# Kernel optimization log

Hardware: AMD Instinct MI355X
Metric: run time of the kernel (lower is better)

Reference implementation:

```python
import jax, jax.numpy as jnp
import numpy as np
from jax.scipy.special import logsumexp

TEMPERATURE = 0.1
BETA = 0.999
EPS = 1e-8
HARD_K = 10  # min(num_classes // 4, 10) with num_classes = 1000


def _l2norm(x, axis=-1):
    return x * jax.lax.rsqrt(jnp.sum(x * x, axis=axis, keepdims=True) + 1e-24)


def setup_inputs() -> dict:
    key = jax.random.key(0)
    k1, k2, k3, k4, k5 = jax.random.split(key, 5)
    B, D, C, M = 4096, 1024, 1000, 32768
    return {
        "image_features": jax.random.normal(k1, (B, D), dtype=jnp.float32),
        "prompts": jax.random.normal(k2, (C, D), dtype=jnp.float32),
        "labels": jax.random.randint(k3, (B, C), 0, 2, dtype=jnp.int32),
        "memory_features": jax.random.normal(k4, (M, D), dtype=jnp.float32),
        "memory_labels": jax.random.randint(k5, (M, C), 0, 2, dtype=jnp.int32),
        "mem_ptr": 16384,
    }


def reference(image_features, prompts, labels, memory_features, memory_labels, mem_ptr):
    B, D = image_features.shape
    C = prompts.shape[0]
    labels_f = labels.astype(jnp.float32)

    # z_img = F.normalize(image_features)
    z_img = _l2norm(image_features, axis=1)

    # class weights (effective-number reweighting), computed from this batch's labels
    counts = labels_f.sum(axis=0)                              # [C]
    effective_num = 1.0 - jnp.power(jnp.float32(BETA), counts)
    weights = (1.0 - BETA) / (effective_num + EPS)
    weights = weights / jnp.sum(weights) * C                   # [C]

    # memory bank update (detached write of current batch at ptr), then use [:ptr+B]
    mem_f = memory_features.at[mem_ptr:mem_ptr + B].set(jax.lax.stop_gradient(z_img))
    mem_l = memory_labels.at[mem_ptr:mem_ptr + B].set(labels)
    used = mem_ptr + B  # static

    enhanced_features = jnp.concatenate([z_img, mem_f[:used]], axis=0)     # [N, D]
    enhanced_labels = jnp.concatenate([labels_f, mem_l[:used].astype(jnp.float32)], axis=0)  # [N, C]

    z_prompts = _l2norm(prompts, axis=1)                       # [C, D]
    sim = (enhanced_features @ z_prompts.T) / TEMPERATURE      # [N, C]

    pos_mask = enhanced_labels > 0                             # [N, C]

    # hard negatives: top-K similarities among negatives define the keep threshold
    sim_for_neg = jnp.where(pos_mask, -jnp.inf, sim)
    hard_neg_vals, _ = jax.lax.top_k(sim_for_neg, HARD_K)      # [N, K]
    min_hard_neg = hard_neg_vals[:, -1:]                       # [N, 1]
    neg_mask = (~pos_mask) & (sim >= min_hard_neg)
    full_mask = pos_mask | neg_mask

    lse = logsumexp(jnp.where(full_mask, sim, -jnp.inf), axis=1)  # [N]
    log_prob = sim - lse[:, None]                              # [N, C]

    posf = pos_mask.astype(sim.dtype)
    pos_w = posf * weights[None, :]                            # [N, C]
    weight_sums = pos_w.sum(axis=1)                            # [N]
    loss_num = (pos_w * (-log_prob)).sum(axis=1)               # [N]

    valid = weight_sums > 0
    loss_per_sample = jnp.where(valid, loss_num / (weight_sums + EPS), 0.0)
    n_valid = jnp.maximum(valid.sum(), 1)
    attr_loss = loss_per_sample.sum() / n_valid.astype(sim.dtype)
    # single attribute -> total_loss / num_valid_attrs == attr_loss
    return attr_loss
```

## Files before the change

### kernel.cpp

```cpp
#include <hip/hip_runtime.h>
#include <math.h>

#define BN    4096
#define DD    1024
#define CC    1000
#define MM    32768
#define ROWS_CAP 32768


#define NGROUP_A 512
#define NGROUP_B 16
#define NCOUNT   512
#define NBITS    512

#define NSUB 32

typedef __attribute__((ext_vector_type(8))) int   int8v;
typedef __attribute__((ext_vector_type(16))) float f32x16;

__device__ __forceinline__ float wave_sum_f(float v) {
#pragma unroll
  for (int off = 32; off >= 1; off >>= 1) v += __shfl_xor(v, off, 64);
  return v;
}

__device__ __forceinline__ int pack4(float a, float b, float c, float d) {
  int p = __builtin_amdgcn_cvt_pk_fp8_f32(a, b, 0, false);
  p = __builtin_amdgcn_cvt_pk_fp8_f32(c, d, p, true);
  return p;
}

__device__ __forceinline__ void gload16(const unsigned char* g, unsigned char* l) {
  __builtin_amdgcn_global_load_lds(
      (const __attribute__((address_space(1))) unsigned int*)g,
      (__attribute__((address_space(3))) unsigned int*)l, 16, 0, 0);
}

__device__ __forceinline__ void ins10(float* t, float v) {
#pragma unroll
  for (int i = 9; i >= 1; --i) t[i] = __builtin_amdgcn_fmed3f(v, t[i - 1], t[i]);
  t[0] = fmaxf(t[0], v);
}

__global__ __launch_bounds__(256) void conv_kernel(const float* __restrict__ img,
                                                   const float* __restrict__ prompts,
                                                   const float* __restrict__ mem,
                                                   const int* __restrict__ memptr,
                                                   unsigned char* __restrict__ A,
                                                   unsigned char* __restrict__ B,
                                                   const int* __restrict__ labels,
                                                   const int* __restrict__ mlabels,
                                                   int* __restrict__ counts,
                                                   unsigned* __restrict__ bitmask) {
  const int blk = blockIdx.x;
  const int t = threadIdx.x;
  const int lane = t & 63;
  const int wid = t >> 6;
  const int nrows = BN + memptr[0];
  const int padded = (nrows + 127) & ~127;

  if (blk >= NGROUP_A + NGROUP_B + NCOUNT) {
    const int bi = blk - (NGROUP_A + NGROUP_B + NCOUNT);
    const int rowBase = bi * 64;
    if (rowBase >= padded) return;
    for (int i = 0; i < 16; ++i) {
      const int row = rowBase + wid * 16 + i;
      if (row >= padded) continue;
      unsigned bits = 0;
      if (row < nrows) {
        const int* lr = (row < BN) ? labels + (size_t)row * CC
                                   : mlabels + (size_t)(row - BN) * CC;
        const int cbase = lane * 16;
#pragma unroll
        for (int g = 0; g < 4; ++g) {
          int c = cbase + g * 4;
          int4 l4;
          if (c + 3 < CC) l4 = *(const int4*)(lr + c);
          else {
            l4.x = (c < CC) ? lr[c] : 0;
            l4.y = (c + 1 < CC) ? lr[c + 1] : 0;
            l4.z = (c + 2 < CC) ? lr[c + 2] : 0;
            l4.w = (c + 3 < CC) ? lr[c + 3] : 0;
          }
          unsigned m = 0;
          if (l4.x > 0) m |= 1u;
          if (l4.y > 0) m |= 2u;
          if (l4.z > 0) m |= 4u;
          if (l4.w > 0) m |= 8u;
          bits |= m << (g * 4);
        }
      }
      unsigned pair = __shfl_xor(bits, 1, 64);
      if (!(lane & 1)) bitmask[(size_t)row * 32 + (lane >> 1)] = bits | (pair << 16);
    }
    return;
  }

  if (blk >= NGROUP_A + NGROUP_B) {
    const int ci = blk - (NGROUP_A + NGROUP_B);
    const int c = (ci & 3) * 256 + t;
    if (c >= CC) return;
    const int b0 = (ci >> 2) * 32;
    int s = 0;
#pragma unroll
    for (int b = 0; b < 32; ++b) s += labels[(size_t)(b0 + b) * CC + c];
    atomicAdd(&counts[c], s);
    return;
  }

  __shared__ unsigned char tile[65536];

  const bool isB = (blk >= NGROUP_A);
  const int g = isB ? (blk - NGROUP_A) : blk;
  const int rowBase = g * 64;
  if (!isB && rowBase >= padded) return;

  unsigned char* dstBase = (isB ? B : A)
      + (size_t)(rowBase >> 7) * 131072 + (size_t)(rowBase & 64) * 16;

  for (int i = 0; i < 16; ++i) {
    const int r = wid * 16 + i;
    const int row = rowBase + r;
    const float* src = nullptr;
    float esc = 1.0f;
    bool needNorm = false;
    if (isB) {
      if (row < CC) { src = prompts + (size_t)row * DD; needNorm = true; esc = 10.0f; }
    } else {
      if (row < BN)         { src = img + (size_t)row * DD; needNorm = true; }
      else if (row < nrows) { src = mem + (size_t)(row - BN) * DD; }
    }
    int4 o = {0, 0, 0, 0};
    if (src) {
      const float4* s4 = (const float4*)src + lane * 4;
      float4 a = s4[0], b = s4[1], c = s4[2], d = s4[3];
      float sc = esc;
      if (needNorm) {
        float ss = a.x * a.x + a.y * a.y + a.z * a.z + a.w * a.w
                 + b.x * b.x + b.y * b.y + b.z * b.z + b.w * b.w
                 + c.x * c.x + c.y * c.y + c.z * c.z + c.w * c.w
                 + d.x * d.x + d.y * d.y + d.z * d.z + d.w * d.w;
        ss = wave_sum_f(ss);
        sc = esc * rsqrtf(ss + 1e-24f);
      }
      o.x = pack4(a.x * sc, a.y * sc, a.z * sc, a.w * sc);
      o.y = pack4(b.x * sc, b.y * sc, b.z * sc, b.w * sc);
      o.z = pack4(c.x * sc, c.y * sc, c.z * sc, c.w * sc);
      o.w = pack4(d.x * sc, d.y * sc, d.z * sc, d.w * sc);
    }
    *(int4*)(tile + lane * 1024 + (((r + lane) & 63) << 4)) = o;
  }
  __syncthreads();

#pragma unroll
  for (int p = 0; p < 16; ++p) {
    const int ochunk = p * 256 + t;
    const int kc = ochunk >> 6;
    const int rl = ochunk & 63;
    int4 v = *(const int4*)(tile + kc * 1024 + (((rl + kc) & 63) << 4));
    *(int4*)(dstBase + (size_t)kc * 2048 + rl * 16) = v;
  }
}

__global__ __launch_bounds__(512) void gemm_fused(
    const unsigned char* __restrict__ A, const unsigned char* __restrict__ Bm,
    const unsigned* __restrict__ bitmask, const int* __restrict__ counts,
    const int* __restrict__ memptr, float* __restrict__ partials) {
  const int f = blockIdx.x;
  const int x = f & 7;
  const int s = f >> 3;
  const int cb = s & 7;
  const int rt = (s >> 3) * 8 + x;

  const int nrows = BN + memptr[0];
  const int row0 = rt * 128;
  if (row0 >= nrows) return;
  const int c0 = cb * 128;

  __shared__ unsigned char As[2][16384];
  __shared__ unsigned char Bs[2][16384];
  __shared__ unsigned posbits[128][4];
  __shared__ float wcol[128];
  __shared__ float wpart[8];

  const int t = threadIdx.x;
  const int lane = t & 63;
  const int wid = t >> 6;
  const int wm = (wid >> 1) * 32;
  const int wn = (wid & 1) * 64;
  const int q = lane >> 5;
  const int rr = lane & 31;

  const unsigned char* gaT = A + (size_t)row0 * DD;
  const unsigned char* gbT = Bm + (size_t)c0 * DD;

#pragma unroll
  for (int p = 0; p < 2; ++p) {
    gload16(gaT + p * 8192 + t * 16, As[0] + p * 8192 + t * 16);
    gload16(gbT + p * 8192 + t * 16, Bs[0] + p * 8192 + t * 16);
  }

  {
    float wv[2];
    float accw = 0.f;
#pragma unroll
    for (int i = 0; i < 2; ++i) {
      int c = t + i * 512;
      float w = 0.f;
      if (c < CC) {
        float cnt = (float)counts[c];
        float en = 1.0f - expf(cnt * logf(0.999f));
        w = (1.0f - 0.999f) / (en + 1e-8f);
      }
      wv[i] = w;
      accw += w;
    }
    float sw = wave_sum_f(accw);
    if (lane == 0) wpart[wid] = sw;
    if (t < 128) {
      const int4 bm = *(const int4*)(bitmask + (size_t)(row0 + t) * 32 + cb * 4);
      posbits[t][0] = bm.x; posbits[t][1] = bm.y;
      posbits[t][2] = bm.z; posbits[t][3] = bm.w;
    }
    __syncthreads();
    float tot = 0.f;
#pragma unroll
    for (int i = 0; i < 8; ++i) tot += wpart[i];
    float scw = (float)CC / tot;
#pragma unroll
    for (int i = 0; i < 2; ++i) {
      int c = t + i * 512;
      if (c >= c0 && c < c0 + 128) wcol[c - c0] = wv[i] * scw;
    }
  }

  f32x16 acc[2] = {};

  int cur = 0;
  for (int it = 0; it < 8; ++it) {
    if (it < 7) {
      const size_t kb = (size_t)(it + 1) * 16384;
#pragma unroll
      for (int p = 0; p < 2; ++p) {
        gload16(gaT + kb + p * 8192 + t * 16, As[cur ^ 1] + p * 8192 + t * 16);
        gload16(gbT + kb + p * 8192 + t * 16, Bs[cur ^ 1] + p * 8192 + t * 16);
      }
    }
#pragma unroll
    for (int h = 0; h < 2; ++h) {
      const int kc = h * 4 + q * 2;
      int8v af, bfv[2];
      {
        const unsigned char* pa = As[cur] + kc * 2048 + (wm + rr) * 16;
        int4 lo4 = *(const int4*)pa;
        int4 hi4 = *(const int4*)(pa + 2048);
        af[0] = lo4.x; af[1] = lo4.y; af[2] = lo4.z; af[3] = lo4.w;
        af[4] = hi4.x; af[5] = hi4.y; af[6] = hi4.z; af[7] = hi4.w;
      }
#pragma unroll
      for (int ni = 0; ni < 2; ++ni) {
        const unsigned char* pb = Bs[cur] + kc * 2048 + (wn + ni * 32 + rr) * 16;
        int4 lo4 = *(const int4*)pb;
        int4 hi4 = *(const int4*)(pb + 2048);
        bfv[ni][0] = lo4.x; bfv[ni][1] = lo4.y; bfv[ni][2] = lo4.z; bfv[ni][3] = lo4.w;
        bfv[ni][4] = hi4.x; bfv[ni][5] = hi4.y; bfv[ni][6] = hi4.z; bfv[ni][7] = hi4.w;
      }
#pragma unroll
      for (int ni = 0; ni < 2; ++ni)
        acc[ni] = __builtin_amdgcn_mfma_scale_f32_32x32x64_f8f6f4(
            bfv[ni], af, acc[ni], 0, 0, 0, 127, 0, 127);
    }
    __syncthreads();
    cur ^= 1;
  }

  const int cl = lane & 31;
  const int rl = wm + cl;
  const int row_g = row0 + rl;
  const int sub = cb * 4 + (wid & 1) * 2 + q;

  float t10[10];
#pragma unroll
  for (int i = 0; i < 10; ++i) t10[i] = -INFINITY;
  float m = -INFINITY, ssum = 0.f, wsum = 0.f, wsim = 0.f;
#pragma unroll
  for (int ni = 0; ni < 2; ++ni) {
    const unsigned bits = posbits[rl][(wid & 1) * 2 + ni];
    f32x16 v = acc[ni];
    float pq = -INFINITY;
    unsigned pb = 0;
#pragma unroll
    for (int reg = 0; reg < 16; ++reg) {
      const int ci = (reg & 3) + 8 * (reg >> 2) + 4 * q;
      const int cg = c0 + wn + ni * 32 + ci;
      const float val = v[reg];
      const bool cvalid = (cg < CC);
      const bool pos = cvalid && ((bits >> ci) & 1u);
      if (pos) {
        float w = wcol[wn + ni * 32 + ci];
        wsum += w;
        wsim += w * val;
        pq = fmaxf(pq, val);
        pb |= 1u << reg;
      }
      ins10(t10, (cvalid && !pos) ? val : -INFINITY);
    }
    if (pb) {
      float ps = 0.f;
#pragma unroll
      for (int reg = 0; reg < 16; ++reg)
        ps += expf(((pb >> reg) & 1u) ? (v[reg] - pq) : -INFINITY);
      float m2 = fmaxf(m, pq);
      ssum = ssum * expf(m - m2) + ps * expf(pq - m2);
      m = m2;
    }
  }
  float* pp = partials + (size_t)sub * ROWS_CAP + row_g;
#pragma unroll
  for (int k = 0; k < 10; ++k) pp[(size_t)k * NSUB * ROWS_CAP] = t10[k];
  pp[(size_t)10 * NSUB * ROWS_CAP] = m;
  pp[(size_t)11 * NSUB * ROWS_CAP] = ssum;
  pp[(size_t)12 * NSUB * ROWS_CAP] = wsum;
  pp[(size_t)13 * NSUB * ROWS_CAP] = wsim;
}

__global__ __launch_bounds__(256) void merge_kernel(const float* __restrict__ partials,
                                                    const int* __restrict__ memptr,
                                                    float* __restrict__ blk_lps,
                                                    float* __restrict__ blk_val) {
  const int t = threadIdx.x;
  const int lane = t & 63;
  const int half = lane >> 5;
  const int row = blockIdx.x * 128 + (t >> 6) * 32 + (lane & 31);
  const int nrows = BN + memptr[0];

  float t10[10];
#pragma unroll
  for (int i = 0; i < 10; ++i) t10[i] = -INFINITY;
  float Mp = -INFINITY, psum = 0.f, wsum = 0.f, wsim = 0.f;

  if (row < nrows) {
    for (int sub = half * 16; sub < half * 16 + 16; ++sub) {
      const float* pp = partials + (size_t)sub * ROWS_CAP + row;
#pragma unroll
      for (int j = 0; j < 10; ++j) {
        float v = pp[(size_t)j * NSUB * ROWS_CAP];
        ins10(t10, v);
      }
      float pm = pp[(size_t)10 * NSUB * ROWS_CAP];
      float ps = pp[(size_t)11 * NSUB * ROWS_CAP];
      wsum += pp[(size_t)12 * NSUB * ROWS_CAP];
      wsim += pp[(size_t)13 * NSUB * ROWS_CAP];
      if (ps > 0.f) {
        float m2 = fmaxf(Mp, pm);
        psum = psum * expf(Mp - m2) + ps * expf(pm - m2);
        Mp = m2;
      }
    }
  }

  float o10[10];
#pragma unroll
  for (int j = 0; j < 10; ++j) o10[j] = __shfl_xor(t10[j], 32, 64);
#pragma unroll
  for (int j = 0; j < 10; ++j) ins10(t10, o10[j]);
  float pm2 = __shfl_xor(Mp, 32, 64);
  float ps2 = __shfl_xor(psum, 32, 64);
  float w2  = __shfl_xor(wsum, 32, 64);
  float ws2 = __shfl_xor(wsim, 32, 64);
  if (ps2 > 0.f) {
    float m2 = fmaxf(Mp, pm2);
    psum = psum * expf(Mp - m2) + ps2 * expf(pm2 - m2);
    Mp = m2;
  }
  wsum += w2;
  wsim += ws2;

  float cl = 0.f, cv = 0.f;
  if (row < nrows && half == 0) {
    const float M = fmaxf(Mp, t10[0]);
    float esum = 0.f;
#pragma unroll
    for (int j = 0; j < 10; ++j) esum += expf(t10[j] - M);
    if (psum > 0.f) esum += psum * expf(Mp - M);
    const float lse = M + logf(esum);
    const bool valid = (wsum > 0.f);
    const float lps = valid ? (wsum * lse - wsim) / (wsum + 1e-8f) : 0.f;
    const float mult = (row < BN) ? 2.f : 1.f;
    cl = mult * lps;
    cv = valid ? mult : 0.f;
  }
  cl = wave_sum_f(cl);
  cv = wave_sum_f(cv);
  __shared__ float p1[4], p2[4];
  if (lane == 0) { p1[t >> 6] = cl; p2[t >> 6] = cv; }
  __syncthreads();
  if (t == 0) {
    blk_lps[blockIdx.x] = p1[0] + p1[1] + p1[2] + p1[3];
    blk_val[blockIdx.x] = p2[0] + p2[1] + p2[2] + p2[3];
  }
}

__global__ __launch_bounds__(256) void reduce_kernel(const float* __restrict__ blk_lps,
                                                     const float* __restrict__ blk_val,
                                                     float* __restrict__ out) {
  const int t = threadIdx.x;
  float a = wave_sum_f(blk_lps[t]);
  float b = wave_sum_f(blk_val[t]);
  __shared__ float p1[4], p2[4];
  if ((t & 63) == 0) { p1[t >> 6] = a; p2[t >> 6] = b; }
  __syncthreads();
  if (t == 0) {
    float A = p1[0] + p1[1] + p1[2] + p1[3];
    float B = p2[0] + p2[1] + p2[2] + p2[3];
    out[0] = A / fmaxf(B, 1.0f);
  }
}

extern "C" void kernel_launch(void* const* d_in, const int* in_sizes, int n_in,
                              void* d_out, int out_size, void* d_ws, size_t ws_size,
                              hipStream_t stream) {
  const float* img     = (const float*)d_in[0];
  const float* prompts = (const float*)d_in[1];
  const int*   labels  = (const int*)d_in[2];
  const float* mem     = (const float*)d_in[3];
  const int*   mlabels = (const int*)d_in[4];
  const int*   memptr  = (const int*)d_in[5];
  float* out = (float*)d_out;
  char* ws = (char*)d_ws;

  int*      counts  = (int*)(ws + 0);
  float*    blk_lps = (float*)(ws + 8192);
  float*    blk_val = (float*)(ws + 12288);
  unsigned* bitmask = (unsigned*)(ws + 270336);
  unsigned char* Bf8 = (unsigned char*)(ws + 4464640);
  unsigned char* Af8 = (unsigned char*)(ws + 5513216);
  float* partials = (float*)(ws + 5513216 + (size_t)ROWS_CAP * DD);

  hipMemsetAsync(ws, 0, 4096, stream);

  conv_kernel<<<NGROUP_A + NGROUP_B + NCOUNT + NBITS, 256, 0, stream>>>(
      img, prompts, mem, memptr, Af8, Bf8, labels, mlabels, counts, bitmask);

  gemm_fused<<<8 * (ROWS_CAP / 128), 512, 0, stream>>>(
      Af8, Bf8, bitmask, counts, memptr, partials);

  merge_kernel<<<ROWS_CAP / 128, 256, 0, stream>>>(partials, memptr, blk_lps, blk_val);

  reduce_kernel<<<1, 256, 0, stream>>>(blk_lps, blk_val, out);
}
```

Before: 392.4 us.

## Prefetch two K-stages ahead in GEMM and pre-merge column halves in-wave

The GEMM main loop now issues loads two stages ahead, using explicit vmcnt waits and raw s_barriers in place of __syncthreads. This is meant to let global-to-LDS loads overlap the MFMA work more fully. The epilogue merges the two q-halves of each wave with shuffles before writing, which halves the partials buffer (NSUB 32→16) and the write traffic. The merge kernel then does one row per thread over 16 subs, and the reduce kernel shrinks to match, at the cost of a fragile hand-tuned wait count.

Measured after the change: 397.7 us. Within noise of the previous version (+1.3%).

```diff
diff --git a/kernel.cpp b/kernel.cpp
--- a/kernel.cpp
+++ b/kernel.cpp
@@ -13,7 +13,7 @@
 #define NCOUNT   512
 #define NBITS    512
 
-#define NSUB 32
+#define NSUB 16
 
 typedef __attribute__((ext_vector_type(8))) int   int8v;
 typedef __attribute__((ext_vector_type(16))) float f32x16;
@@ -199,6 +199,11 @@
     gload16(gaT + p * 8192 + t * 16, As[0] + p * 8192 + t * 16);
     gload16(gbT + p * 8192 + t * 16, Bs[0] + p * 8192 + t * 16);
   }
+#pragma unroll
+  for (int p = 0; p < 2; ++p) {
+    gload16(gaT + 16384 + p * 8192 + t * 16, As[1] + p * 8192 + t * 16);
+    gload16(gbT + 16384 + p * 8192 + t * 16, Bs[1] + p * 8192 + t * 16);
+  }
 
   {
     float wv[2];
@@ -238,14 +243,11 @@
 
   int cur = 0;
   for (int it = 0; it < 8; ++it) {
-    if (it < 7) {
-      const size_t kb = (size_t)(it + 1) * 16384;
-#pragma unroll
-      for (int p = 0; p < 2; ++p) {
-        gload16(gaT + kb + p * 8192 + t * 16, As[cur ^ 1] + p * 8192 + t * 16);
-        gload16(gbT + kb + p * 8192 + t * 16, Bs[cur ^ 1] + p * 8192 + t * 16);
-      }
-    }
+    if (it == 7) asm volatile("s_waitcnt vmcnt(0)" ::: "memory");
+    else         asm volatile("s_waitcnt vmcnt(4)" ::: "memory");
+    __builtin_amdgcn_sched_barrier(0);
+    __builtin_amdgcn_s_barrier();
+    __builtin_amdgcn_sched_barrier(0);
 #pragma unroll
     for (int h = 0; h < 2; ++h) {
       const int kc = h * 4 + q * 2;
@@ -270,14 +272,24 @@
         acc[ni] = __builtin_amdgcn_mfma_scale_f32_32x32x64_f8f6f4(
             bfv[ni], af, acc[ni], 0, 0, 0, 127, 0, 127);
     }
-    __syncthreads();
+    __builtin_amdgcn_sched_barrier(0);
+    __builtin_amdgcn_s_barrier();
+    __builtin_amdgcn_sched_barrier(0);
+    if (it + 2 < 8) {
+      const size_t kb = (size_t)(it + 2) * 16384;
+#pragma unroll
+      for (int p = 0; p < 2; ++p) {
+        gload16(gaT + kb + p * 8192 + t * 16, As[cur] + p * 8192 + t * 16);
+        gload16(gbT + kb + p * 8192 + t * 16, Bs[cur] + p * 8192 + t * 16);
+      }
+    }
     cur ^= 1;
   }
 
   const int cl = lane & 31;
   const int rl = wm + cl;
   const int row_g = row0 + rl;
-  const int sub = cb * 4 + (wid & 1) * 2 + q;
+  const int wnb = wid & 1;
 
   float t10[10];
 #pragma unroll
@@ -285,7 +297,7 @@
   float m = -INFINITY, ssum = 0.f, wsum = 0.f, wsim = 0.f;
 #pragma unroll
   for (int ni = 0; ni < 2; ++ni) {
-    const unsigned bits = posbits[rl][(wid & 1) * 2 + ni];
+    const unsigned bits = posbits[rl][wnb * 2 + ni];
     f32x16 v = acc[ni];
     float pq = -INFINITY;
     unsigned pb = 0;
@@ -315,13 +327,36 @@
       m = m2;
     }
   }
-  float* pp = partials + (size_t)sub * ROWS_CAP + row_g;
-#pragma unroll
-  for (int k = 0; k < 10; ++k) pp[(size_t)k * NSUB * ROWS_CAP] = t10[k];
-  pp[(size_t)10 * NSUB * ROWS_CAP] = m;
-  pp[(size_t)11 * NSUB * ROWS_CAP] = ssum;
-  pp[(size_t)12 * NSUB * ROWS_CAP] = wsum;
-  pp[(size_t)13 * NSUB * ROWS_CAP] = wsim;
+
+  {
+    float o10[10];
+#pragma unroll
+    for (int j = 0; j < 10; ++j) o10[j] = __shfl_xor(t10[j], 32, 64);
+#pragma unroll
+    for (int j = 0; j < 10; ++j) ins10(t10, o10[j]);
+    float pm2 = __shfl_xor(m, 32, 64);
+    float ps2 = __shfl_xor(ssum, 32, 64);
+    float w2  = __shfl_xor(wsum, 32, 64);
+    float ws2 = __shfl_xor(wsim, 32, 64);
+    if (ps2 > 0.f) {
+      float m2 = fmaxf(m, pm2);
+      ssum = ssum * expf(m - m2) + ps2 * expf(pm2 - m2);
+      m = m2;
+    }
+    wsum += w2;
+    wsim += ws2;
+  }
+
+  if (q == 0) {
+    const int sub = cb * 2 + wnb;
+    float* pp = partials + (size_t)sub * ROWS_CAP + row_g;
+#pragma unroll
+    for (int k = 0; k < 10; ++k) pp[(size_t)k * NSUB * ROWS_CAP] = t10[k];
+    pp[(size_t)10 * NSUB * ROWS_CAP] = m;
+    pp[(size_t)11 * NSUB * ROWS_CAP] = ssum;
+    pp[(size_t)12 * NSUB * ROWS_CAP] = wsum;
+    pp[(size_t)13 * NSUB * ROWS_CAP] = wsim;
+  }
 }
 
 __global__ __launch_bounds__(256) void merge_kernel(const float* __restrict__ partials,
@@ -329,24 +364,19 @@
                                                     float* __restrict__ blk_lps,
                                                     float* __restrict__ blk_val) {
   const int t = threadIdx.x;
-  const int lane = t & 63;
-  const int half = lane >> 5;
-  const int row = blockIdx.x * 128 + (t >> 6) * 32 + (lane & 31);
+  const int row = blockIdx.x * 256 + t;
   const int nrows = BN + memptr[0];
 
-  float t10[10];
-#pragma unroll
-  for (int i = 0; i < 10; ++i) t10[i] = -INFINITY;
-  float Mp = -INFINITY, psum = 0.f, wsum = 0.f, wsim = 0.f;
-
+  float cl = 0.f, cv = 0.f;
   if (row < nrows) {
-    for (int sub = half * 16; sub < half * 16 + 16; ++sub) {
+    float t10[10];
+#pragma unroll
+    for (int i = 0; i < 10; ++i) t10[i] = -INFINITY;
+    float Mp = -INFINITY, psum = 0.f, wsum = 0.f, wsim = 0.f;
+    for (int sub = 0; sub < NSUB; ++sub) {
       const float* pp = partials + (size_t)sub * ROWS_CAP + row;
 #pragma unroll
-      for (int j = 0; j < 10; ++j) {
-        float v = pp[(size_t)j * NSUB * ROWS_CAP];
-        ins10(t10, v);
-      }
+      for (int j = 0; j < 10; ++j) ins10(t10, pp[(size_t)j * NSUB * ROWS_CAP]);
       float pm = pp[(size_t)10 * NSUB * ROWS_CAP];
       float ps = pp[(size_t)11 * NSUB * ROWS_CAP];
       wsum += pp[(size_t)12 * NSUB * ROWS_CAP];
@@ -357,27 +387,6 @@
         Mp = m2;
       }
     }
-  }
-
-  float o10[10];
-#pragma unroll
-  for (int j = 0; j < 10; ++j) o10[j] = __shfl_xor(t10[j], 32, 64);
-#pragma unroll
-  for (int j = 0; j < 10; ++j) ins10(t10, o10[j]);
-  float pm2 = __shfl_xor(Mp, 32, 64);
-  float ps2 = __shfl_xor(psum, 32, 64);
-  float w2  = __shfl_xor(wsum, 32, 64);
-  float ws2 = __shfl_xor(wsim, 32, 64);
-  if (ps2 > 0.f) {
-    float m2 = fmaxf(Mp, pm2);
-    psum = psum * expf(Mp - m2) + ps2 * expf(pm2 - m2);
-    Mp = m2;
-  }
-  wsum += w2;
-  wsim += ws2;
-
-  float cl = 0.f, cv = 0.f;
-  if (row < nrows && half == 0) {
     const float M = fmaxf(Mp, t10[0]);
     float esum = 0.f;
 #pragma unroll
@@ -393,7 +402,7 @@
   cl = wave_sum_f(cl);
   cv = wave_sum_f(cv);
   __shared__ float p1[4], p2[4];
-  if (lane == 0) { p1[t >> 6] = cl; p2[t >> 6] = cv; }
+  if ((t & 63) == 0) { p1[t >> 6] = cl; p2[t >> 6] = cv; }
   __syncthreads();
   if (t == 0) {
     blk_lps[blockIdx.x] = p1[0] + p1[1] + p1[2] + p1[3];
@@ -401,20 +410,16 @@
   }
 }
 
-__global__ __launch_bounds__(256) void reduce_kernel(const float* __restrict__ blk_lps,
+__global__ __launch_bounds__(128) void reduce_kernel(const float* __restrict__ blk_lps,
                                                      const float* __restrict__ blk_val,
                                                      float* __restrict__ out) {
   const int t = threadIdx.x;
   float a = wave_sum_f(blk_lps[t]);
   float b = wave_sum_f(blk_val[t]);
-  __shared__ float p1[4], p2[4];
+  __shared__ float p1[2], p2[2];
   if ((t & 63) == 0) { p1[t >> 6] = a; p2[t >> 6] = b; }
   __syncthreads();
-  if (t == 0) {
-    float A = p1[0] + p1[1] + p1[2] + p1[3];
-    float B = p2[0] + p2[1] + p2[2] + p2[3];
-    out[0] = A / fmaxf(B, 1.0f);
-  }
+  if (t == 0) out[0] = (p1[0] + p1[1]) / fmaxf(p2[0] + p2[1], 1.0f);
 }
 
 extern "C" void kernel_launch(void* const* d_in, const int* in_sizes, int n_in,
@@ -445,7 +450,7 @@
   gemm_fused<<<8 * (ROWS_CAP / 128), 512, 0, stream>>>(
       Af8, Bf8, bitmask, counts, memptr, partials);
 
-  merge_kernel<<<ROWS_CAP / 128, 256, 0, stream>>>(partials, memptr, blk_lps, blk_val);
-
-  reduce_kernel<<<1, 256, 0, stream>>>(blk_lps, blk_val, out);
-}
+  merge_kernel<<<ROWS_CAP / 256, 256, 0, stream>>>(partials, memptr, blk_lps, blk_val);
+
+  reduce_kernel<<<1, 128, 0, stream>>>(blk_lps, blk_val, out);
+}
```
